# Optimization experiments

Hardware: AMD Instinct MI355X
Metric: run time of the kernel (lower is better)

The kernel has to match this reference:

```python
import jax, jax.numpy as jnp
import numpy as np

B, S, D = 2, 4096, 768
H = 12
HD = D // H  # 64


def setup_inputs() -> dict:
    key = jax.random.key(0)
    ks = jax.random.split(key, 6)
    scale = 0.02
    return {
        "x": jax.random.normal(ks[0], (B, S, D), dtype=jnp.float32),
        "w_query": jax.random.normal(ks[1], (D, D), dtype=jnp.float32) * scale,
        "w_key": jax.random.normal(ks[2], (D, D), dtype=jnp.float32) * scale,
        "w_value": jax.random.normal(ks[3], (D, D), dtype=jnp.float32) * scale,
        "w_out": jax.random.normal(ks[4], (D, D), dtype=jnp.float32) * scale,
        "b_out": jax.random.normal(ks[5], (D,), dtype=jnp.float32) * scale,
    }


def reference(x, w_query, w_key, w_value, w_out, b_out):
    b, s, d = x.shape
    # Linear(in, out) applies x @ W.T; weights here stored as [out, in]-equivalent
    # square matrices, so use x @ W.T for parity with torch semantics.
    q = (x @ w_query.T).reshape(b, s, H, HD).transpose(0, 2, 1, 3)  # [b,h,s,hd]
    k = (x @ w_key.T).reshape(b, s, H, HD).transpose(0, 2, 1, 3)
    v = (x @ w_value.T).reshape(b, s, H, HD).transpose(0, 2, 1, 3)

    scores = jnp.einsum("bhqd,bhkd->bhqk", q, k)  # [b,h,s,s]
    causal = jnp.triu(jnp.ones((s, s), dtype=bool), k=1)
    scores = jnp.where(causal, -jnp.inf, scores)
    # original scales AFTER masking: softmax(masked / sqrt(head_dim))
    att = jax.nn.softmax(scores / jnp.sqrt(jnp.float32(HD)), axis=-1)
    # dropout p=0.0 (eval) -> identity
    ctx = jnp.einsum("bhqk,bhkd->bhqd", att, v)  # [b,h,s,hd]
    ctx = ctx.transpose(0, 2, 1, 3).reshape(b, s, d)
    return ctx @ w_out.T + b_out
```

## Files before the change

kernel.cpp:

```cpp
#include <hip/hip_runtime.h>
#include <stdint.h>

typedef unsigned short u16;
typedef __attribute__((ext_vector_type(8))) short bf16x8;
typedef __attribute__((ext_vector_type(4))) float f32x4;

#define MFMA(a,b,c) __builtin_amdgcn_mfma_f32_16x16x32_bf16((a),(b),(c),0,0,0)

static constexpr int S  = 4096;
static constexpr int D  = 768;
static constexpr int H  = 12;
static constexpr int HD = 64;

__device__ __forceinline__ u16 f2b(float f){
  union { float f; unsigned u; } v; v.f = f;
  unsigned r = (v.u + 0x7fffu + ((v.u >> 16) & 1u)) >> 16;
  return (u16)r;
}

__device__ __forceinline__ unsigned pack_bf16_trunc(float a, float b){
  return __builtin_amdgcn_perm(__float_as_uint(b), __float_as_uint(a), 0x07060302u);
}

__device__ __forceinline__ void cp16(const u16* g, u16* l){
  __builtin_amdgcn_global_load_lds(
      (const __attribute__((address_space(1))) unsigned int*)g,
      (__attribute__((address_space(3))) unsigned int*)l, 16, 0, 0);
}

__device__ __forceinline__ bf16x8 quad_transpose(unsigned M0, unsigned M1,
                                                 unsigned M2, unsigned M3){
  auto r0 = __builtin_amdgcn_permlane32_swap(M0, M2, false, false);
  auto r1 = __builtin_amdgcn_permlane32_swap(M1, M3, false, false);
  auto s0 = __builtin_amdgcn_permlane16_swap(r0[0], r0[1], false, false);
  auto s1 = __builtin_amdgcn_permlane16_swap(r1[0], r1[1], false, false);
  union { unsigned u[4]; bf16x8 v; } r;
  r.u[0] = s0[0];
  r.u[1] = s1[0];
  r.u[2] = s0[1];
  r.u[3] = s1[1];
  return r.v;
}

static constexpr int NX4 = (2 * S * D) / 4;
static constexpr int NW4 = (D * D) / 4;
__global__ void castall(const float* __restrict__ x,  const float* __restrict__ wq,
                        const float* __restrict__ wk, const float* __restrict__ wv,
                        const float* __restrict__ wo,
                        u16* __restrict__ xb,  u16* __restrict__ wqb,
                        u16* __restrict__ wkb, u16* __restrict__ wvb,
                        u16* __restrict__ wob){
  int i = blockIdx.x * 256 + threadIdx.x;
  const float* s; u16* d; int off;
  if (i < NX4) { s = x; d = xb; off = i; }
  else {
    int j = i - NX4; int wsel = j / NW4; off = j - wsel * NW4;
    if (wsel >= 4) return;
    s = (wsel == 0) ? wq : (wsel == 1) ? wk : (wsel == 2) ? wv : wo;
    d = (wsel == 0) ? wqb : (wsel == 1) ? wkb : (wsel == 2) ? wvb : wob;
  }
  float4 v = ((const float4*)s)[off];
  uint2 o;
  o.x = (unsigned)f2b(v.x) | ((unsigned)f2b(v.y) << 16);
  o.y = (unsigned)f2b(v.z) | ((unsigned)f2b(v.w) << 16);
  ((uint2*)d)[off] = o;
}

__global__ __launch_bounds__(256, 2) void qkv_gemm(
    const u16* __restrict__ xb, const u16* __restrict__ wq, const u16* __restrict__ wk,
    const u16* __restrict__ wv, u16* __restrict__ Qb, u16* __restrict__ Kb, u16* __restrict__ Vt)
{
  __shared__ __align__(16) u16 As[128 * 64];
  __shared__ __align__(16) u16 Bs[128 * 64];
  const int t = threadIdx.x;
  const int mblk = blockIdx.x, nblk = blockIdx.y, z = blockIdx.z;
  const u16* W = (z == 0) ? wq : (z == 1) ? wk : wv;
  const int w = t >> 6, lane = t & 63, quad = lane >> 4, l16 = lane & 15;
  const int wr = w >> 1, wc = w & 1;
  const int l7 = l16 & 7;

  f32x4 acc[4][4];
  #pragma unroll
  for (int i = 0; i < 4; i++)
    #pragma unroll
    for (int j = 0; j < 4; j++) acc[i][j] = (f32x4){0.f, 0.f, 0.f, 0.f};

  int srow[4], schk[4];
  #pragma unroll
  for (int i = 0; i < 4; i++) {
    int s = i * 256 + t;
    srow[i] = s >> 3;
    schk[i] = (s & 7) ^ (srow[i] & 7);
  }
  const u16* gA = xb + (size_t)(mblk * 128) * D;
  const u16* gB = W  + (size_t)(nblk * 128) * D;

  for (int k0 = 0; k0 < D; k0 += 64) {
    __syncthreads();
    #pragma unroll
    for (int i = 0; i < 4; i++) {
      int s = i * 256 + t;
      cp16(gA + (size_t)srow[i] * D + k0 + schk[i] * 8, As + s * 8);
      cp16(gB + (size_t)srow[i] * D + k0 + schk[i] * 8, Bs + s * 8);
    }
    __syncthreads();
    #pragma unroll
    for (int j = 0; j < 2; j++) {
      bf16x8 af[4], bfr[4];
      #pragma unroll
      for (int mt = 0; mt < 4; mt++)
        af[mt]  = *(const bf16x8*)(As + (wr * 64 + mt * 16 + l16) * 64 + ((j * 4 + quad) ^ l7) * 8);
      #pragma unroll
      for (int nt = 0; nt < 4; nt++)
        bfr[nt] = *(const bf16x8*)(Bs + (wc * 64 + nt * 16 + l16) * 64 + ((j * 4 + quad) ^ l7) * 8);
      #pragma unroll
      for (int mt = 0; mt < 4; mt++)
        #pragma unroll
        for (int nt = 0; nt < 4; nt++)
          acc[mt][nt] = MFMA(af[mt], bfr[nt], acc[mt][nt]);
    }
  }

  const float qscale = 0.18033688011112042f;
  #pragma unroll
  for (int mt = 0; mt < 4; mt++) {
    int m0 = mblk * 128 + wr * 64 + mt * 16 + quad * 4;
    #pragma unroll
    for (int nt = 0; nt < 4; nt++) {
      int n = nblk * 128 + wc * 64 + nt * 16 + l16;
      int h = n >> 6, hd = n & 63;
      if (z == 2) {
        int b = m0 >> 12, s0 = m0 & 4095;
        u16* p = Vt + (((size_t)(b * H + h) * HD + hd)) * S + s0;
        uint2 pk;
        pk.x = (unsigned)f2b(acc[mt][nt][0]) | ((unsigned)f2b(acc[mt][nt][1]) << 16);
        pk.y = (unsigned)f2b(acc[mt][nt][2]) | ((unsigned)f2b(acc[mt][nt][3]) << 16);
        *(uint2*)p = pk;
      } else {
        u16* dst = (z == 0) ? Qb : Kb;
        float sc = (z == 0) ? qscale : 1.0f;
        #pragma unroll
        for (int r = 0; r < 4; r++) {
          int m = m0 + r; int b = m >> 12, s = m & 4095;
          dst[((size_t)(b * H + h) * S + s) * HD + hd] = f2b(acc[mt][nt][r] * sc);
        }
      }
    }
  }
}

__global__ __launch_bounds__(256, 2) void attn(
    const u16* __restrict__ Qb, const u16* __restrict__ Kb,
    const u16* __restrict__ Vt, u16* __restrict__ ctx)
{
  __shared__ __align__(16) u16 Ks[128 * 64];
  __shared__ __align__(16) u16 Vts[64 * 128];
  __shared__ float Lbuf[2][4][16];
  const int t = threadIdx.x, w = t >> 6, lane = t & 63, quad = lane >> 4, l16 = lane & 15;
  const int l7 = l16 & 7;
  const int wq = w >> 1, wk = w & 1;
  const int bh = blockIdx.x;
  const int qtile = 31 - (int)blockIdx.y;
  const int q0 = qtile * 128;
  const u16* Qh = Qb + (size_t)bh * S * HD;
  const u16* Kh = Kb + (size_t)bh * S * HD;
  const u16* Vh = Vt + (size_t)bh * S * HD;
  const int b = bh / H, h = bh % H;

  bf16x8 qf[4][2];
  #pragma unroll
  for (int qt = 0; qt < 4; qt++)
    #pragma unroll
    for (int ksh = 0; ksh < 2; ksh++)
      qf[qt][ksh] = *(const bf16x8*)(Qh + (size_t)(q0 + wq * 64 + qt * 16 + l16) * HD + ksh * 32 + quad * 8);

  f32x4 ao[4][4];
  #pragma unroll
  for (int qt = 0; qt < 4; qt++)
    #pragma unroll
    for (int co = 0; co < 4; co++) ao[qt][co] = (f32x4){0.f, 0.f, 0.f, 0.f};
  float lsum[4] = {0.f, 0.f, 0.f, 0.f};

  int krow[4], kchk[4], vrow[4], vchk[4];
  #pragma unroll
  for (int i = 0; i < 4; i++) {
    int s = i * 256 + t;
    krow[i] = s >> 3;  kchk[i] = (s & 7)  ^ (krow[i] & 7);
    vrow[i] = s >> 4;  vchk[i] = (s & 15) ^ (vrow[i] & 15);
  }

  for (int kv0 = 0; kv0 <= q0; kv0 += 128) {
    const bool diag    = (kv0 == q0);
    const bool skipall = diag && (wk > wq);
    const bool mdiag   = diag && (wk == wq);

    __syncthreads();
    #pragma unroll
    for (int i = 0; i < 4; i++) {
      int s = i * 256 + t;
      cp16(Kh + (size_t)(kv0 + krow[i]) * HD + kchk[i] * 8, Ks + s * 8);
      cp16(Vh + (size_t)vrow[i] * S + kv0 + vchk[i] * 8,    Vts + s * 8);
    }
    __syncthreads();

    if (!skipall) {
      #pragma unroll
      for (int g = 0; g < 2; g++) {
        unsigned pA[4][2], pB[4][2];
        #pragma unroll
        for (int ktL = 0; ktL < 2; ktL++) {
          const int kt  = g * 2 + ktL;
          const int krw = wk * 64 + kt * 16 + l16;
          bf16x8 kf0 = *(const bf16x8*)(Ks + krw * 64 + ((0 + quad) ^ l7) * 8);
          bf16x8 kf1 = *(const bf16x8*)(Ks + krw * 64 + ((4 + quad) ^ l7) * 8);
          #pragma unroll
          for (int qt = 0; qt < 4; qt++) {
            f32x4 s0 = (f32x4){0.f, 0.f, 0.f, 0.f};
            s0 = MFMA(kf0, qf[qt][0], s0);
            s0 = MFMA(kf1, qf[qt][1], s0);
            if (mdiag) {
              const int qoff = (qt - kt) * 16 + l16;
              #pragma unroll
              for (int r = 0; r < 4; r++)
                s0[r] = (quad * 4 + r > qoff) ? -1e30f : s0[r];
            }
            float p0 = __builtin_amdgcn_exp2f(s0[0]);
            float p1 = __builtin_amdgcn_exp2f(s0[1]);
            float p2 = __builtin_amdgcn_exp2f(s0[2]);
            float p3 = __builtin_amdgcn_exp2f(s0[3]);
            lsum[qt] += (p0 + p1) + (p2 + p3);
            pA[qt][ktL] = pack_bf16_trunc(p0, p1);
            pB[qt][ktL] = pack_bf16_trunc(p2, p3);
          }
        }
        bf16x8 pf[4];
        #pragma unroll
        for (int qt = 0; qt < 4; qt++)
          pf[qt] = quad_transpose(pA[qt][0], pB[qt][0], pA[qt][1], pB[qt][1]);
        #pragma unroll
        for (int co = 0; co < 4; co++) {
          const int vrw = co * 16 + l16;
          bf16x8 vf = *(const bf16x8*)(Vts + vrw * 128 + ((wk * 8 + g * 4 + quad) ^ (vrw & 15)) * 8);
          #pragma unroll
          for (int qt = 0; qt < 4; qt++)
            ao[qt][co] = MFMA(vf, pf[qt], ao[qt][co]);
        }
      }
    }
  }

  #pragma unroll
  for (int qt = 0; qt < 4; qt++) {
    float v = lsum[qt];
    v += __shfl_xor(v, 16, 64);
    v += __shfl_xor(v, 32, 64);
    lsum[qt] = v;
  }

  __syncthreads();
  float* red = wq ? (float*)Vts : (float*)Ks;
  if (wk == 1) {
    #pragma unroll
    for (int qt = 0; qt < 4; qt++)
      #pragma unroll
      for (int co = 0; co < 4; co++)
        *(f32x4*)(red + ((qt * 4 + co) * 64 + lane) * 4) = ao[qt][co];
    if (lane < 16) {
      #pragma unroll
      for (int qt = 0; qt < 4; qt++) Lbuf[wq][qt][lane] = lsum[qt];
    }
  }
  __syncthreads();
  if (wk == 0) {
    #pragma unroll
    for (int qt = 0; qt < 4; qt++) {
      float tot = lsum[qt] + Lbuf[wq][qt][l16];
      float inv = 1.0f / tot;
      int token = b * S + q0 + wq * 64 + qt * 16 + l16;
      #pragma unroll
      for (int co = 0; co < 4; co++) {
        f32x4 pr = *(const f32x4*)(red + ((qt * 4 + co) * 64 + lane) * 4);
        f32x4 sv = ao[qt][co] + pr;
        uint2 pk;
        pk.x = (unsigned)f2b(sv[0] * inv) | ((unsigned)f2b(sv[1] * inv) << 16);
        pk.y = (unsigned)f2b(sv[2] * inv) | ((unsigned)f2b(sv[3] * inv) << 16);
        *(uint2*)(ctx + (size_t)token * D + h * HD + co * 16 + quad * 4) = pk;
      }
    }
  }
}

__global__ __launch_bounds__(256, 2) void out_gemm(
    const u16* __restrict__ ctx, const u16* __restrict__ wo,
    const float* __restrict__ bias, float* __restrict__ out)
{
  __shared__ __align__(16) u16 As[128 * 64];
  __shared__ __align__(16) u16 Bs[128 * 64];
  const int t = threadIdx.x;
  const int mblk = blockIdx.x, nblk = blockIdx.y;
  const int w = t >> 6, lane = t & 63, quad = lane >> 4, l16 = lane & 15;
  const int wr = w >> 1, wc = w & 1;
  const int l7 = l16 & 7;

  f32x4 acc[4][4];
  #pragma unroll
  for (int i = 0; i < 4; i++)
    #pragma unroll
    for (int j = 0; j < 4; j++) acc[i][j] = (f32x4){0.f, 0.f, 0.f, 0.f};

  int srow[4], schk[4];
  #pragma unroll
  for (int i = 0; i < 4; i++) {
    int s = i * 256 + t;
    srow[i] = s >> 3;
    schk[i] = (s & 7) ^ (srow[i] & 7);
  }
  const u16* gA = ctx + (size_t)(mblk * 128) * D;
  const u16* gB = wo  + (size_t)(nblk * 128) * D;

  for (int k0 = 0; k0 < D; k0 += 64) {
    __syncthreads();
    #pragma unroll
    for (int i = 0; i < 4; i++) {
      int s = i * 256 + t;
      cp16(gA + (size_t)srow[i] * D + k0 + schk[i] * 8, As + s * 8);
      cp16(gB + (size_t)srow[i] * D + k0 + schk[i] * 8, Bs + s * 8);
    }
    __syncthreads();
    #pragma unroll
    for (int j = 0; j < 2; j++) {
      bf16x8 af[4], bfr[4];
      #pragma unroll
      for (int mt = 0; mt < 4; mt++)
        af[mt]  = *(const bf16x8*)(As + (wr * 64 + mt * 16 + l16) * 64 + ((j * 4 + quad) ^ l7) * 8);
      #pragma unroll
      for (int nt = 0; nt < 4; nt++)
        bfr[nt] = *(const bf16x8*)(Bs + (wc * 64 + nt * 16 + l16) * 64 + ((j * 4 + quad) ^ l7) * 8);
      #pragma unroll
      for (int mt = 0; mt < 4; mt++)
        #pragma unroll
        for (int nt = 0; nt < 4; nt++)
          acc[mt][nt] = MFMA(af[mt], bfr[nt], acc[mt][nt]);
    }
  }

  #pragma unroll
  for (int mt = 0; mt < 4; mt++) {
    int m0 = mblk * 128 + wr * 64 + mt * 16 + quad * 4;
    #pragma unroll
    for (int nt = 0; nt < 4; nt++) {
      int n = nblk * 128 + wc * 64 + nt * 16 + l16;
      float bv = bias[n];
      #pragma unroll
      for (int r = 0; r < 4; r++)
        out[(size_t)(m0 + r) * D + n] = acc[mt][nt][r] + bv;
    }
  }
}

extern "C" void kernel_launch(void* const* d_in, const int* in_sizes, int n_in,
                              void* d_out, int out_size, void* d_ws, size_t ws_size,
                              hipStream_t stream) {
  const float* x    = (const float*)d_in[0];
  const float* wq   = (const float*)d_in[1];
  const float* wk   = (const float*)d_in[2];
  const float* wv   = (const float*)d_in[3];
  const float* wo   = (const float*)d_in[4];
  const float* bo   = (const float*)d_in[5];
  float* out = (float*)d_out;

  u16* ws = (u16*)d_ws;
  const size_t NX = (size_t)2 * S * D;
  const size_t NW = (size_t)D * D;
  u16* xb  = ws;
  u16* wqb = ws + NX;
  u16* wkb = wqb + NW;
  u16* wvb = wkb + NW;
  u16* wob = wvb + NW;
  u16* Qb  = wob + NW;
  u16* Kb  = Qb + NX;
  u16* Vt  = Kb + NX;
  u16* ctx = xb;

  const int total4 = NX4 + 4 * NW4;
  castall<<<(total4 + 255) / 256, 256, 0, stream>>>(x, wq, wk, wv, wo, xb, wqb, wkb, wvb, wob);

  qkv_gemm<<<dim3(64, 6, 3), 256, 0, stream>>>(xb, wqb, wkb, wvb, Qb, Kb, Vt);
  attn<<<dim3(24, 32), 256, 0, stream>>>(Qb, Kb, Vt, ctx);
  out_gemm<<<dim3(64, 6), 256, 0, stream>>>(ctx, wob, bo, out);
}
```

Before: 224.3 us.

## Make attention persistent with atomic work queue and double-buffered K/V loads

The attention kernel becomes persistent: 512 blocks pull (head, query-tile) units from a global atomic counter, longest tiles first. The counter is reset in the cast kernel. K/V tiles are now double-buffered in LDS so the next tile's async global-to-LDS copy overlaps the current tile's MFMA work. This is meant to fix the load imbalance of causal tiles and hide load latency. In exchange, LDS use doubles, which may limit occupancy, and each unit adds an atomic round trip plus a barrier.

```diff
diff --git a/kernel.cpp b/kernel.cpp
--- a/kernel.cpp
+++ b/kernel.cpp
@@ -11,6 +11,7 @@
 static constexpr int D  = 768;
 static constexpr int H  = 12;
 static constexpr int HD = 64;
+static constexpr unsigned NUNITS = 24 * 32;
 
 __device__ __forceinline__ u16 f2b(float f){
   union { float f; unsigned u; } v; v.f = f;
@@ -49,7 +50,8 @@
                         const float* __restrict__ wo,
                         u16* __restrict__ xb,  u16* __restrict__ wqb,
                         u16* __restrict__ wkb, u16* __restrict__ wvb,
-                        u16* __restrict__ wob){
+                        u16* __restrict__ wob, unsigned* __restrict__ ctr){
+  if (blockIdx.x == 0 && threadIdx.x == 0) *ctr = 0u;
   int i = blockIdx.x * 256 + threadIdx.x;
   const float* s; u16* d; int off;
   if (i < NX4) { s = x; d = xb; off = i; }
@@ -151,35 +153,15 @@
 
 __global__ __launch_bounds__(256, 2) void attn(
     const u16* __restrict__ Qb, const u16* __restrict__ Kb,
-    const u16* __restrict__ Vt, u16* __restrict__ ctx)
+    const u16* __restrict__ Vt, u16* __restrict__ ctx, unsigned* __restrict__ ctr)
 {
-  __shared__ __align__(16) u16 Ks[128 * 64];
-  __shared__ __align__(16) u16 Vts[64 * 128];
+  __shared__ __align__(16) u16 Ks[2][128 * 64];
+  __shared__ __align__(16) u16 Vts[2][64 * 128];
   __shared__ float Lbuf[2][4][16];
+  __shared__ unsigned s_unit;
   const int t = threadIdx.x, w = t >> 6, lane = t & 63, quad = lane >> 4, l16 = lane & 15;
   const int l7 = l16 & 7;
   const int wq = w >> 1, wk = w & 1;
-  const int bh = blockIdx.x;
-  const int qtile = 31 - (int)blockIdx.y;
-  const int q0 = qtile * 128;
-  const u16* Qh = Qb + (size_t)bh * S * HD;
-  const u16* Kh = Kb + (size_t)bh * S * HD;
-  const u16* Vh = Vt + (size_t)bh * S * HD;
-  const int b = bh / H, h = bh % H;
-
-  bf16x8 qf[4][2];
-  #pragma unroll
-  for (int qt = 0; qt < 4; qt++)
-    #pragma unroll
-    for (int ksh = 0; ksh < 2; ksh++)
-      qf[qt][ksh] = *(const bf16x8*)(Qh + (size_t)(q0 + wq * 64 + qt * 16 + l16) * HD + ksh * 32 + quad * 8);
-
-  f32x4 ao[4][4];
-  #pragma unroll
-  for (int qt = 0; qt < 4; qt++)
-    #pragma unroll
-    for (int co = 0; co < 4; co++) ao[qt][co] = (f32x4){0.f, 0.f, 0.f, 0.f};
-  float lsum[4] = {0.f, 0.f, 0.f, 0.f};
 
   int krow[4], kchk[4], vrow[4], vchk[4];
   #pragma unroll
@@ -189,102 +171,144 @@
     vrow[i] = s >> 4;  vchk[i] = (s & 15) ^ (vrow[i] & 15);
   }
 
-  for (int kv0 = 0; kv0 <= q0; kv0 += 128) {
-    const bool diag    = (kv0 == q0);
-    const bool skipall = diag && (wk > wq);
-    const bool mdiag   = diag && (wk == wq);
-
-    __syncthreads();
+  for (;;) {
+    if (t == 0) s_unit = atomicAdd(ctr, 1u);
+    __syncthreads();
+    const unsigned u = s_unit;
+    if (u >= NUNITS) break;
+    const int bh    = (int)(u % 24u);
+    const int qtile = 31 - (int)(u / 24u);
+    const int q0 = qtile * 128;
+    const u16* Qh = Qb + (size_t)bh * S * HD;
+    const u16* Kh = Kb + (size_t)bh * S * HD;
+    const u16* Vh = Vt + (size_t)bh * S * HD;
+    const int b = bh / H, h = bh % H;
+
+    bf16x8 qf[4][2];
+    #pragma unroll
+    for (int qt = 0; qt < 4; qt++)
+      #pragma unroll
+      for (int ksh = 0; ksh < 2; ksh++)
+        qf[qt][ksh] = *(const bf16x8*)(Qh + (size_t)(q0 + wq * 64 + qt * 16 + l16) * HD + ksh * 32 + quad * 8);
+
+    f32x4 ao[4][4];
+    #pragma unroll
+    for (int qt = 0; qt < 4; qt++)
+      #pragma unroll
+      for (int co = 0; co < 4; co++) ao[qt][co] = (f32x4){0.f, 0.f, 0.f, 0.f};
+    float lsum[4] = {0.f, 0.f, 0.f, 0.f};
+
     #pragma unroll
     for (int i = 0; i < 4; i++) {
       int s = i * 256 + t;
-      cp16(Kh + (size_t)(kv0 + krow[i]) * HD + kchk[i] * 8, Ks + s * 8);
-      cp16(Vh + (size_t)vrow[i] * S + kv0 + vchk[i] * 8,    Vts + s * 8);
-    }
-    __syncthreads();
-
-    if (!skipall) {
-      #pragma unroll
-      for (int g = 0; g < 2; g++) {
-        unsigned pA[4][2], pB[4][2];
-        #pragma unroll
-        for (int ktL = 0; ktL < 2; ktL++) {
-          const int kt  = g * 2 + ktL;
-          const int krw = wk * 64 + kt * 16 + l16;
-          bf16x8 kf0 = *(const bf16x8*)(Ks + krw * 64 + ((0 + quad) ^ l7) * 8);
-          bf16x8 kf1 = *(const bf16x8*)(Ks + krw * 64 + ((4 + quad) ^ l7) * 8);
+      cp16(Kh + (size_t)krow[i] * HD + kchk[i] * 8, &Ks[0][0] + s * 8);
+      cp16(Vh + (size_t)vrow[i] * S + vchk[i] * 8,  &Vts[0][0] + s * 8);
+    }
+
+    int cur = 0;
+    for (int kv0 = 0; kv0 <= q0; kv0 += 128) {
+      const bool diag    = (kv0 == q0);
+      const bool skipall = diag && (wk > wq);
+      const bool mdiag   = diag && (wk == wq);
+
+      __syncthreads();
+
+      if (!diag) {
+        const int kn = kv0 + 128;
+        #pragma unroll
+        for (int i = 0; i < 4; i++) {
+          int s = i * 256 + t;
+          cp16(Kh + (size_t)(kn + krow[i]) * HD + kchk[i] * 8, &Ks[cur ^ 1][0] + s * 8);
+          cp16(Vh + (size_t)vrow[i] * S + kn + vchk[i] * 8,    &Vts[cur ^ 1][0] + s * 8);
+        }
+      }
+
+      if (!skipall) {
+        const u16* Kc = &Ks[cur][0];
+        const u16* Vc = &Vts[cur][0];
+        #pragma unroll
+        for (int g = 0; g < 2; g++) {
+          unsigned pA[4][2], pB[4][2];
           #pragma unroll
-          for (int qt = 0; qt < 4; qt++) {
-            f32x4 s0 = (f32x4){0.f, 0.f, 0.f, 0.f};
-            s0 = MFMA(kf0, qf[qt][0], s0);
-            s0 = MFMA(kf1, qf[qt][1], s0);
-            if (mdiag) {
-              const int qoff = (qt - kt) * 16 + l16;
-              #pragma unroll
-              for (int r = 0; r < 4; r++)
-                s0[r] = (quad * 4 + r > qoff) ? -1e30f : s0[r];
+          for (int ktL = 0; ktL < 2; ktL++) {
+            const int kt  = g * 2 + ktL;
+            const int krw = wk * 64 + kt * 16 + l16;
+            bf16x8 kf0 = *(const bf16x8*)(Kc + krw * 64 + ((0 + quad) ^ l7) * 8);
+            bf16x8 kf1 = *(const bf16x8*)(Kc + krw * 64 + ((4 + quad) ^ l7) * 8);
+            #pragma unroll
+            for (int qt = 0; qt < 4; qt++) {
+              f32x4 s0 = (f32x4){0.f, 0.f, 0.f, 0.f};
+              s0 = MFMA(kf0, qf[qt][0], s0);
+              s0 = MFMA(kf1, qf[qt][1], s0);
+              if (mdiag) {
+                const int qoff = (qt - kt) * 16 + l16;
+                #pragma unroll
+                for (int r = 0; r < 4; r++)
+                  s0[r] = (quad * 4 + r > qoff) ? -1e30f : s0[r];
+              }
+              float p0 = __builtin_amdgcn_exp2f(s0[0]);
+              float p1 = __builtin_amdgcn_exp2f(s0[1]);
+              float p2 = __builtin_amdgcn_exp2f(s0[2]);
+              float p3 = __builtin_amdgcn_exp2f(s0[3]);
+              lsum[qt] += (p0 + p1) + (p2 + p3);
+              pA[qt][ktL] = pack_bf16_trunc(p0, p1);
+              pB[qt][ktL] = pack_bf16_trunc(p2, p3);
             }
-            float p0 = __builtin_amdgcn_exp2f(s0[0]);
-            float p1 = __builtin_amdgcn_exp2f(s0[1]);
-            float p2 = __builtin_amdgcn_exp2f(s0[2]);
-            float p3 = __builtin_amdgcn_exp2f(s0[3]);
-            lsum[qt] += (p0 + p1) + (p2 + p3);
-            pA[qt][ktL] = pack_bf16_trunc(p0, p1);
-            pB[qt][ktL] = pack_bf16_trunc(p2, p3);
+          }
+          bf16x8 pf[4];
+          #pragma unroll
+          for (int qt = 0; qt < 4; qt++)
+            pf[qt] = quad_transpose(pA[qt][0], pB[qt][0], pA[qt][1], pB[qt][1]);
+          #pragma unroll
+          for (int co = 0; co < 4; co++) {
+            const int vrw = co * 16 + l16;
+            bf16x8 vf = *(const bf16x8*)(Vc + vrw * 128 + ((wk * 8 + g * 4 + quad) ^ (vrw & 15)) * 8);
+            #pragma unroll
+            for (int qt = 0; qt < 4; qt++)
+              ao[qt][co] = MFMA(vf, pf[qt], ao[qt][co]);
           }
         }
-        bf16x8 pf[4];
-        #pragma unroll
-        for (int qt = 0; qt < 4; qt++)
-          pf[qt] = quad_transpose(pA[qt][0], pB[qt][0], pA[qt][1], pB[qt][1]);
+      }
+      cur ^= 1;
+    }
+
+    #pragma unroll
+    for (int qt = 0; qt < 4; qt++) {
+      float v = lsum[qt];
+      v += __shfl_xor(v, 16, 64);
+      v += __shfl_xor(v, 32, 64);
+      lsum[qt] = v;
+    }
+
+    __syncthreads();
+    float* red = wq ? (float*)&Vts[0][0] : (float*)&Ks[0][0];
+    if (wk == 1) {
+      #pragma unroll
+      for (int qt = 0; qt < 4; qt++)
+        #pragma unroll
+        for (int co = 0; co < 4; co++)
+          *(f32x4*)(red + ((qt * 4 + co) * 64 + lane) * 4) = ao[qt][co];
+      if (lane < 16) {
+        #pragma unroll
+        for (int qt = 0; qt < 4; qt++) Lbuf[wq][qt][lane] = lsum[qt];
+      }
+    }
+    __syncthreads();
+    if (wk == 0) {
+      #pragma unroll
+      for (int qt = 0; qt < 4; qt++) {
+        float tot = lsum[qt] + Lbuf[wq][qt][l16];
+        float inv = 1.0f / tot;
+        int token = b * S + q0 + wq * 64 + qt * 16 + l16;
         #pragma unroll
         for (int co = 0; co < 4; co++) {
-          const int vrw = co * 16 + l16;
-          bf16x8 vf = *(const bf16x8*)(Vts + vrw * 128 + ((wk * 8 + g * 4 + quad) ^ (vrw & 15)) * 8);
-          #pragma unroll
-          for (int qt = 0; qt < 4; qt++)
-            ao[qt][co] = MFMA(vf, pf[qt], ao[qt][co]);
+          f32x4 pr = *(const f32x4*)(red + ((qt * 4 + co) * 64 + lane) * 4);
+          f32x4 sv = ao[qt][co] + pr;
+          uint2 pk;
+          pk.x = (unsigned)f2b(sv[0] * inv) | ((unsigned)f2b(sv[1] * inv) << 16);
+          pk.y = (unsigned)f2b(sv[2] * inv) | ((unsigned)f2b(sv[3] * inv) << 16);
+          *(uint2*)(ctx + (size_t)token * D + h * HD + co * 16 + quad * 4) = pk;
         }
-      }
-    }
-  }
-
-  #pragma unroll
-  for (int qt = 0; qt < 4; qt++) {
-    float v = lsum[qt];
-    v += __shfl_xor(v, 16, 64);
-    v += __shfl_xor(v, 32, 64);
-    lsum[qt] = v;
-  }
-
-  __syncthreads();
-  float* red = wq ? (float*)Vts : (float*)Ks;
-  if (wk == 1) {
-    #pragma unroll
-    for (int qt = 0; qt < 4; qt++)
-      #pragma unroll
-      for (int co = 0; co < 4; co++)
-        *(f32x4*)(red + ((qt * 4 + co) * 64 + lane) * 4) = ao[qt][co];
-    if (lane < 16) {
-      #pragma unroll
-      for (int qt = 0; qt < 4; qt++) Lbuf[wq][qt][lane] = lsum[qt];
-    }
-  }
-  __syncthreads();
-  if (wk == 0) {
-    #pragma unroll
-    for (int qt = 0; qt < 4; qt++) {
-      float tot = lsum[qt] + Lbuf[wq][qt][l16];
-      float inv = 1.0f / tot;
-      int token = b * S + q0 + wq * 64 + qt * 16 + l16;
-      #pragma unroll
-      for (int co = 0; co < 4; co++) {
-        f32x4 pr = *(const f32x4*)(red + ((qt * 4 + co) * 64 + lane) * 4);
-        f32x4 sv = ao[qt][co] + pr;
-        uint2 pk;
-        pk.x = (unsigned)f2b(sv[0] * inv) | ((unsigned)f2b(sv[1] * inv) << 16);
-        pk.y = (unsigned)f2b(sv[2] * inv) | ((unsigned)f2b(sv[3] * inv) << 16);
-        *(uint2*)(ctx + (size_t)token * D + h * HD + co * 16 + quad * 4) = pk;
       }
     }
   }
@@ -381,11 +405,12 @@
   u16* Kb  = Qb + NX;
   u16* Vt  = Kb + NX;
   u16* ctx = xb;
+  unsigned* ctr = (unsigned*)(Vt + NX);
 
   const int total4 = NX4 + 4 * NW4;
-  castall<<<(total4 + 255) / 256, 256, 0, stream>>>(x, wq, wk, wv, wo, xb, wqb, wkb, wvb, wob);
+  castall<<<(total4 + 255) / 256, 256, 0, stream>>>(x, wq, wk, wv, wo, xb, wqb, wkb, wvb, wob, ctr);
 
   qkv_gemm<<<dim3(64, 6, 3), 256, 0, stream>>>(xb, wqb, wkb, wvb, Qb, Kb, Vt);
-  attn<<<dim3(24, 32), 256, 0, stream>>>(Qb, Kb, Vt, ctx);
+  attn<<<dim3(512), 256, 0, stream>>>(Qb, Kb, Vt, ctx, ctr);
   out_gemm<<<dim3(64, 6), 256, 0, stream>>>(ctx, wob, bo, out);
 }
```

Result: slower. 232.8 us (+3.8%).

## Double-buffer K/V tiles in attention and flatten grid ordering

Applied to the files above, without the earlier changes.

Splits the attention kernel's K and V shared-memory tiles into two buffers, so the next KV tile is loaded asynchronously while the current one is being computed. Synchronisation uses manual vmcnt waits and s_barrier instead of a pair of __syncthreads around each load. The 2D grid becomes a 1D grid that walks all heads within a query tile before moving on, longest tiles first. This doubles LDS use to about 64KB per block, which may limit occupancy, and it depends on the hand-written waitcnt being correct for the cp16 loads.

```diff
diff --git a/kernel.cpp b/kernel.cpp
--- a/kernel.cpp
+++ b/kernel.cpp
@@ -153,14 +153,16 @@
     const u16* __restrict__ Qb, const u16* __restrict__ Kb,
     const u16* __restrict__ Vt, u16* __restrict__ ctx)
 {
-  __shared__ __align__(16) u16 Ks[128 * 64];
-  __shared__ __align__(16) u16 Vts[64 * 128];
+  __shared__ __align__(16) u16 Ks[2][128 * 64];
+  __shared__ __align__(16) u16 Vts[2][64 * 128];
   __shared__ float Lbuf[2][4][16];
   const int t = threadIdx.x, w = t >> 6, lane = t & 63, quad = lane >> 4, l16 = lane & 15;
   const int l7 = l16 & 7;
   const int wq = w >> 1, wk = w & 1;
-  const int bh = blockIdx.x;
-  const int qtile = 31 - (int)blockIdx.y;
+
+  const int p   = (int)blockIdx.x;
+  const int bh    = p % 24;
+  const int qtile = 31 - p / 24;
   const int q0 = qtile * 128;
   const u16* Qh = Qb + (size_t)bh * S * HD;
   const u16* Kh = Kb + (size_t)bh * S * HD;
@@ -173,6 +175,7 @@
     #pragma unroll
     for (int ksh = 0; ksh < 2; ksh++)
       qf[qt][ksh] = *(const bf16x8*)(Qh + (size_t)(q0 + wq * 64 + qt * 16 + l16) * HD + ksh * 32 + quad * 8);
+  asm volatile("s_waitcnt vmcnt(0)" ::: "memory");
 
   f32x4 ao[4][4];
   #pragma unroll
@@ -189,21 +192,31 @@
     vrow[i] = s >> 4;  vchk[i] = (s & 15) ^ (vrow[i] & 15);
   }
 
-  for (int kv0 = 0; kv0 <= q0; kv0 += 128) {
-    const bool diag    = (kv0 == q0);
+  auto stage = [&](int kv, int d){
+    #pragma unroll
+    for (int i = 0; i < 4; i++) {
+      int s = i * 256 + t;
+      cp16(Kh + (size_t)(kv + krow[i]) * HD + kchk[i] * 8, &Ks[d][0] + s * 8);
+      cp16(Vh + (size_t)vrow[i] * S + kv + vchk[i] * 8,    &Vts[d][0] + s * 8);
+    }
+  };
+
+  const int nt = q0 / 128 + 1;
+  stage(0, 0);
+
+  for (int i = 0; i < nt; ++i) {
+    const int cur = i & 1;
+    const bool diag = (i == nt - 1);
+    if (!diag) stage((i + 1) * 128, cur ^ 1);
+    if (!diag) asm volatile("s_waitcnt vmcnt(8)\ns_barrier" ::: "memory");
+    else       asm volatile("s_waitcnt vmcnt(0)\ns_barrier" ::: "memory");
+
     const bool skipall = diag && (wk > wq);
     const bool mdiag   = diag && (wk == wq);
 
-    __syncthreads();
-    #pragma unroll
-    for (int i = 0; i < 4; i++) {
-      int s = i * 256 + t;
-      cp16(Kh + (size_t)(kv0 + krow[i]) * HD + kchk[i] * 8, Ks + s * 8);
-      cp16(Vh + (size_t)vrow[i] * S + kv0 + vchk[i] * 8,    Vts + s * 8);
-    }
-    __syncthreads();
-
     if (!skipall) {
+      const u16* Kc = &Ks[cur][0];
+      const u16* Vc = &Vts[cur][0];
       #pragma unroll
       for (int g = 0; g < 2; g++) {
         unsigned pA[4][2], pB[4][2];
@@ -211,8 +224,8 @@
         for (int ktL = 0; ktL < 2; ktL++) {
           const int kt  = g * 2 + ktL;
           const int krw = wk * 64 + kt * 16 + l16;
-          bf16x8 kf0 = *(const bf16x8*)(Ks + krw * 64 + ((0 + quad) ^ l7) * 8);
-          bf16x8 kf1 = *(const bf16x8*)(Ks + krw * 64 + ((4 + quad) ^ l7) * 8);
+          bf16x8 kf0 = *(const bf16x8*)(Kc + krw * 64 + ((0 + quad) ^ l7) * 8);
+          bf16x8 kf1 = *(const bf16x8*)(Kc + krw * 64 + ((4 + quad) ^ l7) * 8);
           #pragma unroll
           for (int qt = 0; qt < 4; qt++) {
             f32x4 s0 = (f32x4){0.f, 0.f, 0.f, 0.f};
@@ -240,13 +253,14 @@
         #pragma unroll
         for (int co = 0; co < 4; co++) {
           const int vrw = co * 16 + l16;
-          bf16x8 vf = *(const bf16x8*)(Vts + vrw * 128 + ((wk * 8 + g * 4 + quad) ^ (vrw & 15)) * 8);
+          bf16x8 vf = *(const bf16x8*)(Vc + vrw * 128 + ((wk * 8 + g * 4 + quad) ^ (vrw & 15)) * 8);
           #pragma unroll
           for (int qt = 0; qt < 4; qt++)
             ao[qt][co] = MFMA(vf, pf[qt], ao[qt][co]);
         }
       }
     }
+    asm volatile("s_barrier" ::: "memory");
   }
 
   #pragma unroll
@@ -257,8 +271,7 @@
     lsum[qt] = v;
   }
 
-  __syncthreads();
-  float* red = wq ? (float*)Vts : (float*)Ks;
+  float* red = wq ? (float*)&Vts[0][0] : (float*)&Ks[0][0];
   if (wk == 1) {
     #pragma unroll
     for (int qt = 0; qt < 4; qt++)
@@ -386,6 +399,6 @@
   castall<<<(total4 + 255) / 256, 256, 0, stream>>>(x, wq, wk, wv, wo, xb, wqb, wkb, wvb, wob);
 
   qkv_gemm<<<dim3(64, 6, 3), 256, 0, stream>>>(xb, wqb, wkb, wvb, Qb, Kb, Vt);
-  attn<<<dim3(24, 32), 256, 0, stream>>>(Qb, Kb, Vt, ctx);
+  attn<<<dim3(768), 256, 0, stream>>>(Qb, Kb, Vt, ctx);
   out_gemm<<<dim3(64, 6), 256, 0, stream>>>(ctx, wob, bo, out);
 }
```

Result: faster. 215.4 us (-3.9%).
